# Performance work log

Measured on AMD Instinct MI355X. Metric: run time of the kernel, lower is better.

Reference implementation:

```python
import jax, jax.numpy as jnp
import numpy as np

N = 65536            # query points (256x256 image)
G = 2048             # number of gaussian/gabor primitives
K = 8                # top-k wave frequencies per primitive
NUM_TOTAL_FREQ = 128
MAX_FREQ = 128.0


def setup_inputs() -> dict:
    key = jax.random.key(0)
    ks = jax.random.split(key, 7)
    x = jax.random.uniform(ks[0], (N, 2), jnp.float32)
    gaussian_colors = 0.05 * jax.random.normal(ks[1], (G, 3), jnp.float32)
    gaussian_positions = jax.random.uniform(ks[2], (G, 2), jnp.float32)
    gaussian_scales = 3.0 + 0.05 * jax.random.normal(ks[3], (G, 2), jnp.float32)
    gaussian_rotations = jnp.pi * jax.random.uniform(ks[4], (G, 1), jnp.float32)
    topk_wave_coefficients = 0.01 * (2.0 * jax.random.uniform(ks[5], (G, K), jnp.float32) - 1.0)
    topk_wave_indices = jax.random.randint(ks[6], (G, K), 0, NUM_TOTAL_FREQ)
    return {
        "x": x,
        "gaussian_colors": gaussian_colors,
        "gaussian_positions": gaussian_positions,
        "gaussian_scales": gaussian_scales,
        "gaussian_rotations": gaussian_rotations,
        "topk_wave_coefficients": topk_wave_coefficients,
        "topk_wave_indices": topk_wave_indices,
    }


def reference(x, gaussian_colors, gaussian_positions, gaussian_scales,
              gaussian_rotations, topk_wave_coefficients, topk_wave_indices):
    # Dense (unblocked) faithful evaluation of the periodic-primitive splat:
    # out[n] = sum_g color_g * exp(-0.5*((rx*sx)^2+(ry*sy)^2)) * sum_k c_gk*cos(2*pi*f_gk*rx)
    dx = x[:, None, 0] - gaussian_positions[None, :, 0]   # [N, G]
    dy = x[:, None, 1] - gaussian_positions[None, :, 1]   # [N, G]
    th = gaussian_rotations[:, 0]                          # [G]
    c, s = jnp.cos(th), jnp.sin(th)
    rx = c[None, :] * dx + s[None, :] * dy                 # rotated coords [N, G]
    ry = -s[None, :] * dx + c[None, :] * dy
    sx = gaussian_scales[None, :, 0]
    sy = gaussian_scales[None, :, 1]
    env = jnp.exp(-0.5 * ((rx * sx) ** 2 + (ry * sy) ** 2))  # gaussian envelope [N, G]
    # frequency of each selected coefficient: idx * max_freq / num_total_freq
    freqs = topk_wave_indices.astype(jnp.float32) * (MAX_FREQ / NUM_TOTAL_FREQ)  # [G, K]
    two_pi = 2.0 * jnp.pi
    wave = jnp.zeros_like(env)
    for k in range(K):  # small fixed loop -> avoids materializing [N, G, K]
        wave = wave + topk_wave_coefficients[:, k][None, :] * jnp.cos(two_pi * freqs[:, k][None, :] * rx)
    return (env * wave) @ gaussian_colors  # [N, 3]
```

## Files before the change

### kernel.cpp

```cpp
#include <hip/hip_runtime.h>
#include <math.h>

#define G_NUM   2048
#define N_PTS   65536
#define K_FREQ  8
#define REC     32
#define CHUNKS  16
#define G_PER_CHUNK (G_NUM / CHUNKS)
#define PACK_BYTES ((size_t)G_NUM * REC * sizeof(float))
#define PART_FLOATS ((size_t)N_PTS * 3)
#define PART_BYTES  (PART_FLOATS * sizeof(float) * CHUNKS)

typedef float v2f __attribute__((ext_vector_type(2)));

#if __has_builtin(__builtin_amdgcn_cosf)
__device__ __forceinline__ float hw_cos_rev(float p) { return __builtin_amdgcn_cosf(p); }
#else
__device__ __forceinline__ float hw_cos_rev(float p) { return __cosf(6.28318530717958648f * p); }
#endif
#if __has_builtin(__builtin_amdgcn_exp2f)
__device__ __forceinline__ float hw_exp2(float p) { return __builtin_amdgcn_exp2f(p); }
#else
__device__ __forceinline__ float hw_exp2(float p) { return exp2f(p); }
#endif

__device__ __forceinline__ v2f fma2(v2f a, float b, v2f c) {
#if __has_builtin(__builtin_elementwise_fma)
    v2f bb = {b, b};
    return __builtin_elementwise_fma(a, bb, c);
#else
    v2f r; r.x = fmaf(a.x, b, c.x); r.y = fmaf(a.y, b, c.y); return r;
#endif
}
__device__ __forceinline__ v2f fma2v(v2f a, v2f b, v2f c) {
#if __has_builtin(__builtin_elementwise_fma)
    return __builtin_elementwise_fma(a, b, c);
#else
    v2f r; r.x = fmaf(a.x, b.x, c.x); r.y = fmaf(a.y, b.y, c.y); return r;
#endif
}

__global__ __launch_bounds__(256) void pack_kernel(
    const float* __restrict__ colors, const float* __restrict__ pos,
    const float* __restrict__ scales, const float* __restrict__ rot,
    const float* __restrict__ coef,   const int* __restrict__ idx,
    float* __restrict__ pack)
{
    int j = blockIdx.x * blockDim.x + threadIdx.x;
    if (j >= G_NUM) return;
    float th = rot[j];
    float c = cosf(th), s = sinf(th);
    float sx = scales[2 * j], sy = scales[2 * j + 1];
    const float nhl2e = -0.72134752044448170368f;
    float* r = pack + (size_t)j * REC;
    r[0] = pos[2 * j];
    r[1] = pos[2 * j + 1];
    r[2] = c;
    r[3] = s;
    r[4] = nhl2e * sx * sx;
    r[5] = nhl2e * sy * sy;
    r[6] = colors[3 * j];
    r[7] = colors[3 * j + 1];
    r[8] = colors[3 * j + 2];
    r[9] = -s;
#pragma unroll
    for (int k = 0; k < K_FREQ; ++k) {
        r[10 + k] = (float)idx[j * K_FREQ + k];
        r[18 + k] = coef[j * K_FREQ + k];
    }
#pragma unroll
    for (int t = 26; t < REC; ++t) r[t] = 0.0f;
}

template <bool USE_PART>
__global__ __launch_bounds__(256, 8) void periodic2d_kernel(
    const float* __restrict__ x, const float* __restrict__ pack,
    float* __restrict__ dst )
{
    const int t = blockIdx.x * 256 + threadIdx.x;
    const int p0 = t;
    const int p1 = t + N_PTS / 2;
    const float2 q0 = ((const float2*)x)[p0];
    const float2 q1 = ((const float2*)x)[p1];
    const v2f xi = {q0.x, q1.x};
    const v2f yi = {q0.y, q1.y};
    v2f a0 = {0.f, 0.f}, a1 = {0.f, 0.f}, a2 = {0.f, 0.f};
    const float* __restrict__ r = pack + (size_t)(blockIdx.y * G_PER_CHUNK) * REC;
#pragma unroll 2
    for (int j = 0; j < G_PER_CHUNK; ++j, r += REC) {
        const v2f dx = xi - r[0];
        const v2f dy = yi - r[1];
        const v2f rx = fma2(dx, r[2], dy * r[3]);
        const v2f ry = fma2(dx, r[9], dy * r[2]);
        const v2f earg = fma2v(ry * r[5], ry, (rx * r[4]) * rx);
        v2f env; env.x = hw_exp2(earg.x); env.y = hw_exp2(earg.y);
        v2f wave = {0.f, 0.f};
#pragma unroll
        for (int k = 0; k < K_FREQ; ++k) {
            const v2f ph = rx * r[10 + k];
            v2f ck; ck.x = hw_cos_rev(ph.x); ck.y = hw_cos_rev(ph.y);
            wave = fma2(ck, r[18 + k], wave);
        }
        const v2f w = env * wave;
        a0 = fma2(w, r[6], a0);
        a1 = fma2(w, r[7], a1);
        a2 = fma2(w, r[8], a2);
    }
    if (USE_PART) {
        float* o = dst + (size_t)blockIdx.y * PART_FLOATS;
        o[3 * p0 + 0] = a0.x; o[3 * p0 + 1] = a1.x; o[3 * p0 + 2] = a2.x;
        o[3 * p1 + 0] = a0.y; o[3 * p1 + 1] = a1.y; o[3 * p1 + 2] = a2.y;
    } else {
        atomicAdd(&dst[3 * p0 + 0], a0.x);
        atomicAdd(&dst[3 * p0 + 1], a1.x);
        atomicAdd(&dst[3 * p0 + 2], a2.x);
        atomicAdd(&dst[3 * p1 + 0], a0.y);
        atomicAdd(&dst[3 * p1 + 1], a1.y);
        atomicAdd(&dst[3 * p1 + 2], a2.y);
    }
}

__global__ __launch_bounds__(256) void reduce_kernel(
    const float* __restrict__ part, float* __restrict__ out)
{
    const int i = blockIdx.x * 256 + threadIdx.x;
    float s = 0.f;
#pragma unroll
    for (int c = 0; c < CHUNKS; ++c) s += part[(size_t)c * PART_FLOATS + i];
    out[i] = s;
}

extern "C" void kernel_launch(void* const* d_in, const int* in_sizes, int n_in,
                              void* d_out, int out_size, void* d_ws, size_t ws_size,
                              hipStream_t stream)
{
    const float* x      = (const float*)d_in[0];
    const float* colors = (const float*)d_in[1];
    const float* pos    = (const float*)d_in[2];
    const float* scales = (const float*)d_in[3];
    const float* rot    = (const float*)d_in[4];
    const float* coef   = (const float*)d_in[5];
    const int*   idx    = (const int*)d_in[6];
    float* out  = (float*)d_out;
    float* pack = (float*)d_ws;
    float* part = (float*)((char*)d_ws + PACK_BYTES);

    pack_kernel<<<dim3((G_NUM + 255) / 256), 256, 0, stream>>>(
        colors, pos, scales, rot, coef, idx, pack);

    if (ws_size >= PACK_BYTES + PART_BYTES) {
        periodic2d_kernel<true><<<dim3(N_PTS / 512, CHUNKS), 256, 0, stream>>>(
            x, pack, part);
        reduce_kernel<<<dim3((N_PTS * 3) / 256), 256, 0, stream>>>(part, out);
    } else {
        (void)hipMemsetAsync(d_out, 0, (size_t)out_size * sizeof(float), stream);
        periodic2d_kernel<false><<<dim3(N_PTS / 512, CHUNKS), 256, 0, stream>>>(
            x, pack, out);
    }
}
```

Measured before the change: 203.0 us.

## Process four points per thread and fold translation into packed rotation

Each thread now evaluates four query points instead of two, reusing each loaded primitive record across more points and halving the grid. The pack kernel precomputes the rotated translation so rotated coordinates need only FMAs, with no separate subtraction. The reduce kernel is vectorised to float4. This lowers occupancy (launch bound 4) and raises register use in exchange for more instruction-level parallelism and fewer scalar loads.

```diff
diff --git a/kernel.cpp b/kernel.cpp
--- a/kernel.cpp
+++ b/kernel.cpp
@@ -39,6 +39,7 @@
     v2f r; r.x = fmaf(a.x, b.x, c.x); r.y = fmaf(a.y, b.y, c.y); return r;
 #endif
 }
+__device__ __forceinline__ v2f spread(float b) { v2f r = {b, b}; return r; }
 
 __global__ __launch_bounds__(256) void pack_kernel(
     const float* __restrict__ colors, const float* __restrict__ pos,
@@ -50,19 +51,20 @@
     if (j >= G_NUM) return;
     float th = rot[j];
     float c = cosf(th), s = sinf(th);
+    float px = pos[2 * j], py = pos[2 * j + 1];
     float sx = scales[2 * j], sy = scales[2 * j + 1];
     const float nhl2e = -0.72134752044448170368f;
     float* r = pack + (size_t)j * REC;
-    r[0] = pos[2 * j];
-    r[1] = pos[2 * j + 1];
-    r[2] = c;
-    r[3] = s;
-    r[4] = nhl2e * sx * sx;
-    r[5] = nhl2e * sy * sy;
-    r[6] = colors[3 * j];
-    r[7] = colors[3 * j + 1];
-    r[8] = colors[3 * j + 2];
-    r[9] = -s;
+    r[0] = c;
+    r[1] = s;
+    r[2] = -s;
+    r[3] = -(c * px + s * py);
+    r[4] = s * px - c * py;
+    r[5] = nhl2e * sx * sx;
+    r[6] = nhl2e * sy * sy;
+    r[7] = colors[3 * j];
+    r[8] = colors[3 * j + 1];
+    r[9] = colors[3 * j + 2];
 #pragma unroll
     for (int k = 0; k < K_FREQ; ++k) {
         r[10 + k] = (float)idx[j * K_FREQ + k];
@@ -73,50 +75,74 @@
 }
 
 template <bool USE_PART>
-__global__ __launch_bounds__(256, 8) void periodic2d_kernel(
+__global__ __launch_bounds__(256, 4) void periodic2d_kernel(
     const float* __restrict__ x, const float* __restrict__ pack,
     float* __restrict__ dst )
 {
     const int t = blockIdx.x * 256 + threadIdx.x;
     const int p0 = t;
-    const int p1 = t + N_PTS / 2;
+    const int p1 = t + N_PTS / 4;
+    const int p2 = t + N_PTS / 2;
+    const int p3 = t + 3 * (N_PTS / 4);
     const float2 q0 = ((const float2*)x)[p0];
     const float2 q1 = ((const float2*)x)[p1];
-    const v2f xi = {q0.x, q1.x};
-    const v2f yi = {q0.y, q1.y};
-    v2f a0 = {0.f, 0.f}, a1 = {0.f, 0.f}, a2 = {0.f, 0.f};
+    const float2 q2 = ((const float2*)x)[p2];
+    const float2 q3 = ((const float2*)x)[p3];
+    const v2f xiA = {q0.x, q1.x}, yiA = {q0.y, q1.y};
+    const v2f xiB = {q2.x, q3.x}, yiB = {q2.y, q3.y};
+    v2f a0A = {0.f, 0.f}, a1A = {0.f, 0.f}, a2A = {0.f, 0.f};
+    v2f a0B = {0.f, 0.f}, a1B = {0.f, 0.f}, a2B = {0.f, 0.f};
     const float* __restrict__ r = pack + (size_t)(blockIdx.y * G_PER_CHUNK) * REC;
 #pragma unroll 2
     for (int j = 0; j < G_PER_CHUNK; ++j, r += REC) {
-        const v2f dx = xi - r[0];
-        const v2f dy = yi - r[1];
-        const v2f rx = fma2(dx, r[2], dy * r[3]);
-        const v2f ry = fma2(dx, r[9], dy * r[2]);
-        const v2f earg = fma2v(ry * r[5], ry, (rx * r[4]) * rx);
-        v2f env; env.x = hw_exp2(earg.x); env.y = hw_exp2(earg.y);
-        v2f wave = {0.f, 0.f};
+        const float cth = r[0], sth = r[1], nsth = r[2];
+        const float tx = r[3], ty = r[4], A = r[5], B = r[6];
+        const v2f rxA = fma2(xiA, cth, fma2(yiA, sth, spread(tx)));
+        const v2f rxB = fma2(xiB, cth, fma2(yiB, sth, spread(tx)));
+        const v2f ryA = fma2(yiA, cth, fma2(xiA, nsth, spread(ty)));
+        const v2f ryB = fma2(yiB, cth, fma2(xiB, nsth, spread(ty)));
+        const v2f eargA = fma2v(ryA * B, ryA, (rxA * A) * rxA);
+        const v2f eargB = fma2v(ryB * B, ryB, (rxB * A) * rxB);
+        v2f envA, envB;
+        envA.x = hw_exp2(eargA.x); envA.y = hw_exp2(eargA.y);
+        envB.x = hw_exp2(eargB.x); envB.y = hw_exp2(eargB.y);
+        v2f waveA = {0.f, 0.f}, waveB = {0.f, 0.f};
 #pragma unroll
         for (int k = 0; k < K_FREQ; ++k) {
-            const v2f ph = rx * r[10 + k];
-            v2f ck; ck.x = hw_cos_rev(ph.x); ck.y = hw_cos_rev(ph.y);
-            wave = fma2(ck, r[18 + k], wave);
+            const float fk = r[10 + k], ck = r[18 + k];
+            const v2f phA = rxA * fk;
+            const v2f phB = rxB * fk;
+            v2f cA, cB;
+            cA.x = hw_cos_rev(phA.x); cA.y = hw_cos_rev(phA.y);
+            cB.x = hw_cos_rev(phB.x); cB.y = hw_cos_rev(phB.y);
+            waveA = fma2(cA, ck, waveA);
+            waveB = fma2(cB, ck, waveB);
         }
-        const v2f w = env * wave;
-        a0 = fma2(w, r[6], a0);
-        a1 = fma2(w, r[7], a1);
-        a2 = fma2(w, r[8], a2);
+        const v2f wA = envA * waveA;
+        const v2f wB = envB * waveB;
+        a0A = fma2(wA, r[7], a0A);  a0B = fma2(wB, r[7], a0B);
+        a1A = fma2(wA, r[8], a1A);  a1B = fma2(wB, r[8], a1B);
+        a2A = fma2(wA, r[9], a2A);  a2B = fma2(wB, r[9], a2B);
     }
     if (USE_PART) {
         float* o = dst + (size_t)blockIdx.y * PART_FLOATS;
-        o[3 * p0 + 0] = a0.x; o[3 * p0 + 1] = a1.x; o[3 * p0 + 2] = a2.x;
-        o[3 * p1 + 0] = a0.y; o[3 * p1 + 1] = a1.y; o[3 * p1 + 2] = a2.y;
+        o[3 * p0 + 0] = a0A.x; o[3 * p0 + 1] = a1A.x; o[3 * p0 + 2] = a2A.x;
+        o[3 * p1 + 0] = a0A.y; o[3 * p1 + 1] = a1A.y; o[3 * p1 + 2] = a2A.y;
+        o[3 * p2 + 0] = a0B.x; o[3 * p2 + 1] = a1B.x; o[3 * p2 + 2] = a2B.x;
+        o[3 * p3 + 0] = a0B.y; o[3 * p3 + 1] = a1B.y; o[3 * p3 + 2] = a2B.y;
     } else {
-        atomicAdd(&dst[3 * p0 + 0], a0.x);
-        atomicAdd(&dst[3 * p0 + 1], a1.x);
-        atomicAdd(&dst[3 * p0 + 2], a2.x);
-        atomicAdd(&dst[3 * p1 + 0], a0.y);
-        atomicAdd(&dst[3 * p1 + 1], a1.y);
-        atomicAdd(&dst[3 * p1 + 2], a2.y);
+        atomicAdd(&dst[3 * p0 + 0], a0A.x);
+        atomicAdd(&dst[3 * p0 + 1], a1A.x);
+        atomicAdd(&dst[3 * p0 + 2], a2A.x);
+        atomicAdd(&dst[3 * p1 + 0], a0A.y);
+        atomicAdd(&dst[3 * p1 + 1], a1A.y);
+        atomicAdd(&dst[3 * p1 + 2], a2A.y);
+        atomicAdd(&dst[3 * p2 + 0], a0B.x);
+        atomicAdd(&dst[3 * p2 + 1], a1B.x);
+        atomicAdd(&dst[3 * p2 + 2], a2B.x);
+        atomicAdd(&dst[3 * p3 + 0], a0B.y);
+        atomicAdd(&dst[3 * p3 + 1], a1B.y);
+        atomicAdd(&dst[3 * p3 + 2], a2B.y);
     }
 }
 
@@ -124,10 +150,13 @@
     const float* __restrict__ part, float* __restrict__ out)
 {
     const int i = blockIdx.x * 256 + threadIdx.x;
-    float s = 0.f;
+    float4 s = {0.f, 0.f, 0.f, 0.f};
 #pragma unroll
-    for (int c = 0; c < CHUNKS; ++c) s += part[(size_t)c * PART_FLOATS + i];
-    out[i] = s;
+    for (int c = 0; c < CHUNKS; ++c) {
+        const float4 v = ((const float4*)(part + (size_t)c * PART_FLOATS))[i];
+        s.x += v.x; s.y += v.y; s.z += v.z; s.w += v.w;
+    }
+    ((float4*)out)[i] = s;
 }
 
 extern "C" void kernel_launch(void* const* d_in, const int* in_sizes, int n_in,
@@ -149,12 +178,12 @@
         colors, pos, scales, rot, coef, idx, pack);
 
     if (ws_size >= PACK_BYTES + PART_BYTES) {
-        periodic2d_kernel<true><<<dim3(N_PTS / 512, CHUNKS), 256, 0, stream>>>(
+        periodic2d_kernel<true><<<dim3(N_PTS / 1024, CHUNKS), 256, 0, stream>>>(
             x, pack, part);
-        reduce_kernel<<<dim3((N_PTS * 3) / 256), 256, 0, stream>>>(part, out);
+        reduce_kernel<<<dim3((N_PTS * 3 / 4) / 256), 256, 0, stream>>>(part, out);
     } else {
         (void)hipMemsetAsync(d_out, 0, (size_t)out_size * sizeof(float), stream);
-        periodic2d_kernel<false><<<dim3(N_PTS / 512, CHUNKS), 256, 0, stream>>>(
+        periodic2d_kernel<false><<<dim3(N_PTS / 1024, CHUNKS), 256, 0, stream>>>(
             x, pack, out);
     }
 }
```

Result: no change. 203.0 us (-0.0%).
